# Optimization experiments

Hardware: AMD Instinct MI355X
Metric: run time of the kernel (lower is better)

The kernel has to match this reference:

```python
import jax, jax.numpy as jnp
import numpy as np

MASK_VALUE = -1000000.0

def setup_inputs() -> dict:
    key = jax.random.key(0)
    ks = jax.random.split(key, 8)
    B, Lq, Lk = 8, 128, 512
    Dq = Dk = H = Dv = 256
    queries = jax.random.normal(ks[0], (B, Lq, Dq), dtype=jnp.float32)
    keys = jax.random.normal(ks[1], (B, Lk, Dk), dtype=jnp.float32)
    values = jax.random.normal(ks[2], (B, Lk, Dv), dtype=jnp.float32)
    valid_lens = jax.random.randint(ks[3], (B,), 1, Lk + 1).astype(jnp.int32)
    # Learned parameters (stored as (in, out) so x @ W matches torch Linear)
    Wq = jax.random.normal(ks[4], (Dq, H), dtype=jnp.float32) / np.sqrt(Dq)
    Wk = jax.random.normal(ks[5], (Dk, H), dtype=jnp.float32) / np.sqrt(Dk)
    wv = jax.random.normal(ks[6], (H,), dtype=jnp.float32) / np.sqrt(H)
    return {"queries": queries, "keys": keys, "values": values,
            "valid_lens": valid_lens, "Wq": Wq, "Wk": Wk, "wv": wv}

def reference(queries, keys, values, valid_lens, Wq, Wk, wv):
    # projections
    q = jnp.einsum('bqd,dh->bqh', queries, Wq)   # (B, Lq, H)
    k = jnp.einsum('bkd,dh->bkh', keys, Wk)      # (B, Lk, H)
    # additive score: tanh(q_i + k_j) . w_v  -> (B, Lq, Lk)
    features = jnp.tanh(q[:, :, None, :] + k[:, None, :, :])  # (B, Lq, Lk, H)
    scores = jnp.einsum('bqkh,h->bqk', features, wv)
    # masked softmax over k axis; masked positions set to -1e6 (as in torch src)
    Lk = keys.shape[1]
    mask = jnp.arange(Lk)[None, None, :] >= valid_lens[:, None, None]  # (B,1,Lk)
    scores = jnp.where(mask, MASK_VALUE, scores)
    attn = jax.nn.softmax(scores, axis=-1)
    # dropout p=0.0 -> identity
    return jnp.einsum('bqk,bkv->bqv', attn, values)  # (B, Lq, Dv)
```

## Files before the change

### kernel.cpp

```cpp
#include <hip/hip_runtime.h>
#include <hip/hip_bf16.h>


#define SCALE_2LOG2E 2.885390081777927f
#define LOG2E        1.4426950408889634f
#define NEG_BIG     -1.0e30f

__device__ __forceinline__ float fast_exp2(float x) {
#if __has_builtin(__builtin_amdgcn_exp2f)
    return __builtin_amdgcn_exp2f(x);
#else
    return exp2f(x);
#endif
}
__device__ __forceinline__ float fast_rcp(float x) {
#if __has_builtin(__builtin_amdgcn_rcpf)
    return __builtin_amdgcn_rcpf(x);
#else
    return __fdividef(1.0f, x);
#endif
}

__global__ __launch_bounds__(256) void proj_kernel(
    const float* __restrict__ queries, const float* __restrict__ keys,
    const float* __restrict__ Wq, const float* __restrict__ Wk,
    const int* __restrict__ valid_lens,
    float* __restrict__ qproj, float* __restrict__ kproj)
{
    const int mt = blockIdx.y, nt = blockIdx.x;
    const float* X; const float* W; float* P; int row0;
    if (mt < 16) { X = queries; W = Wq; P = qproj; row0 = mt * 64; }
    else {
        const int kr = mt * 64 - 1024;
        const int b = kr >> 9, loc = kr & 511;
        if (loc >= valid_lens[b]) return;
        X = keys; W = Wk; P = kproj; row0 = kr;
    }
    const int t  = threadIdx.x;
    const int tx = t & 15, ty = t >> 4;
    const int ar = t >> 2, ac = t & 3;
    const int br = t >> 4, bc = t & 15;
    const int n0 = nt * 64;

    __shared__ float as[16][68];
    __shared__ float bs[16][68];

    const float* Aptr = X + (size_t)(row0 + ar) * 256 + ac * 4;
    const float* Bptr = W + (size_t)br * 256 + n0 + bc * 4;

    float4 av = *(const float4*)Aptr;
    float4 bv = *(const float4*)Bptr;

    float acc[4][4];
#pragma unroll
    for (int i = 0; i < 4; ++i)
#pragma unroll
        for (int j = 0; j < 4; ++j) acc[i][j] = 0.f;

    for (int ch = 0; ch < 16; ++ch) {
        __syncthreads();
        as[ac * 4 + 0][ar] = av.x;
        as[ac * 4 + 1][ar] = av.y;
        as[ac * 4 + 2][ar] = av.z;
        as[ac * 4 + 3][ar] = av.w;
        *(float4*)&bs[br][bc * 4] = bv;
        __syncthreads();
        if (ch < 15) {
            av = *(const float4*)(Aptr + (ch + 1) * 16);
            bv = *(const float4*)(Bptr + (size_t)(ch + 1) * 16 * 256);
        }
#pragma unroll
        for (int kk = 0; kk < 16; ++kk) {
            const float4 af = *(const float4*)&as[kk][ty * 4];
            const float4 bf = *(const float4*)&bs[kk][tx * 4];
            acc[0][0] += af.x * bf.x; acc[0][1] += af.x * bf.y;
            acc[0][2] += af.x * bf.z; acc[0][3] += af.x * bf.w;
            acc[1][0] += af.y * bf.x; acc[1][1] += af.y * bf.y;
            acc[1][2] += af.y * bf.z; acc[1][3] += af.y * bf.w;
            acc[2][0] += af.z * bf.x; acc[2][1] += af.z * bf.y;
            acc[2][2] += af.z * bf.z; acc[2][3] += af.z * bf.w;
            acc[3][0] += af.w * bf.x; acc[3][1] += af.w * bf.y;
            acc[3][2] += af.w * bf.z; acc[3][3] += af.w * bf.w;
        }
    }
#pragma unroll
    for (int i = 0; i < 4; ++i) {
        float4 o;
        o.x = acc[i][0] * SCALE_2LOG2E; o.y = acc[i][1] * SCALE_2LOG2E;
        o.z = acc[i][2] * SCALE_2LOG2E; o.w = acc[i][3] * SCALE_2LOG2E;
        *(float4*)(P + (size_t)(row0 + ty * 4 + i) * 256 + n0 + tx * 4) = o;
    }
}

__global__ __launch_bounds__(256) void score_kernel(
    const float* __restrict__ qproj,
    const float* __restrict__ kproj,
    const float* __restrict__ wv,
    const int*   __restrict__ valid_lens,
    float* __restrict__ scores)
{
    const int b  = blockIdx.z;
    const int vlen = valid_lens[b];
    const int k0 = blockIdx.x * 16;
    if (k0 >= vlen) return;
    const int q0 = blockIdx.y * 16;
    const int t  = threadIdx.x;

    __shared__ float qs[16][260];
    __shared__ float ks[16][260];
    __shared__ float wl[256];

    {
        const float4* qsrc = (const float4*)(qproj + (size_t)(b * 128 + q0) * 256);
        const float4* ksrc = (const float4*)(kproj + ((size_t)b * 512 + k0) * 256);
        for (int i = t; i < 1024; i += 256) {
            *(float4*)&qs[i >> 6][(i & 63) * 4] = qsrc[i];
            *(float4*)&ks[i >> 6][(i & 63) * 4] = ksrc[i];
        }
        if (t < 64) *(float4*)&wl[t * 4] = ((const float4*)wv)[t];
    }
    __syncthreads();

    const int tx = t & 15, ty = t >> 4;
    float acc = 0.f;
#pragma unroll 8
    for (int h0 = 0; h0 < 256; h0 += 4) {
        const float4 qf = *(const float4*)&qs[ty][h0];
        const float4 kf = *(const float4*)&ks[tx][h0];
        const float4 wf = *(const float4*)&wl[h0];
        float a, r;
        a = qf.x + kf.x; r = fast_rcp(fast_exp2(a) + 1.f);
        acc += wf.x * (1.f - 2.f * r);
        a = qf.y + kf.y; r = fast_rcp(fast_exp2(a) + 1.f);
        acc += wf.y * (1.f - 2.f * r);
        a = qf.z + kf.z; r = fast_rcp(fast_exp2(a) + 1.f);
        acc += wf.z * (1.f - 2.f * r);
        a = qf.w + kf.w; r = fast_rcp(fast_exp2(a) + 1.f);
        acc += wf.w * (1.f - 2.f * r);
    }
    if (k0 + tx < vlen)
        scores[(size_t)(b * 128 + q0 + ty) * 512 + k0 + tx] = acc;
}

__global__ __launch_bounds__(256) void softmax_pv_kernel(
    const float* __restrict__ scores,
    const float* __restrict__ values,
    const int*   __restrict__ valid_lens,
    float* __restrict__ out)
{
    __shared__ float attn[4][512];
    const int b = blockIdx.y, q0 = blockIdx.x * 4;
    const int t = threadIdx.x, w = t >> 6, lane = t & 63;
    const int vlen = valid_lens[b];
    const int row = q0 + w;

    const float* srow = scores + (size_t)(b * 128 + row) * 512;
    float sv[8];
#pragma unroll
    for (int j = 0; j < 8; ++j) {
        const int k = lane + 64 * j;
        sv[j] = (k < vlen) ? srow[k] : NEG_BIG;
    }

    float m = sv[0];
#pragma unroll
    for (int j = 1; j < 8; ++j) m = fmaxf(m, sv[j]);
#pragma unroll
    for (int o = 1; o < 64; o <<= 1) m = fmaxf(m, __shfl_xor(m, o));

    float sum = 0.f;
#pragma unroll
    for (int j = 0; j < 8; ++j) {
        sv[j] = fast_exp2((sv[j] - m) * LOG2E);
        sum += sv[j];
    }
#pragma unroll
    for (int o = 1; o < 64; o <<= 1) sum += __shfl_xor(sum, o);
    const float rs = fast_rcp(sum);

#pragma unroll
    for (int j = 0; j < 8; ++j) attn[w][lane + 64 * j] = sv[j] * rs;

    const float* V = values + (size_t)b * 512 * 256 + lane * 4;
    float4 acc = {0.f, 0.f, 0.f, 0.f};
#pragma unroll 4
    for (int k = 0; k < vlen; ++k) {
        const float a = attn[w][k];
        const float4 v4 = *(const float4*)(V + (size_t)k * 256);
        acc.x += a * v4.x; acc.y += a * v4.y;
        acc.z += a * v4.z; acc.w += a * v4.w;
    }
    *(float4*)(out + (size_t)(b * 128 + row) * 256 + lane * 4) = acc;
}

extern "C" void kernel_launch(void* const* d_in, const int* in_sizes, int n_in,
                              void* d_out, int out_size, void* d_ws, size_t ws_size,
                              hipStream_t stream) {
    const float* queries = (const float*)d_in[0];
    const float* keys    = (const float*)d_in[1];
    const float* values  = (const float*)d_in[2];
    const int*   vlens   = (const int*)  d_in[3];
    const float* Wq      = (const float*)d_in[4];
    const float* Wk      = (const float*)d_in[5];
    const float* wv      = (const float*)d_in[6];
    float* out = (float*)d_out;

    float* qproj  = (float*)d_ws;
    float* kproj  = qproj + 1024 * 256;
    float* scores = kproj + 4096 * 256;

    proj_kernel<<<dim3(4, 80), 256, 0, stream>>>(queries, keys, Wq, Wk,
                                                 vlens, qproj, kproj);
    score_kernel<<<dim3(32, 8, 8), 256, 0, stream>>>(qproj, kproj, wv,
                                                     vlens, scores);
    softmax_pv_kernel<<<dim3(32, 8), 256, 0, stream>>>(scores, values,
                                                       vlens, out);
}
```

Baseline: 148.7 us.

## Hoist tanh affine terms out of score loop and split PV over key halves

In the score kernel, tanh(x) = 1 - 2/(e^{2x}+1) is rearranged so the constant sum of wv is computed once per block with a wave reduction. The inner loop then only accumulates wv*rcp(exp2+1), which saves a few ALU ops per element. The softmax/PV kernel now handles 2 rows per block instead of 4, with two waves per row each covering half the keys, combined through shared memory. It also processes 4 keys per step using vectorized attention reads. This doubles the block count and adds parallelism for the memory-bound PV phase, at the cost of computing each row's softmax twice and adding a block sync.

Measured after the change: 141.5 us. 1.05x faster.

```diff
diff --git a/kernel.cpp b/kernel.cpp
--- a/kernel.cpp
+++ b/kernel.cpp
@@ -121,6 +121,14 @@
     }
     __syncthreads();
 
+    float wsum;
+    {
+        const float4 wq = *(const float4*)&wl[(t & 63) * 4];
+        wsum = wq.x + wq.y + wq.z + wq.w;
+#pragma unroll
+        for (int o = 1; o < 64; o <<= 1) wsum += __shfl_xor(wsum, o);
+    }
+
     const int tx = t & 15, ty = t >> 4;
     float acc = 0.f;
 #pragma unroll 8
@@ -128,18 +136,13 @@
         const float4 qf = *(const float4*)&qs[ty][h0];
         const float4 kf = *(const float4*)&ks[tx][h0];
         const float4 wf = *(const float4*)&wl[h0];
-        float a, r;
-        a = qf.x + kf.x; r = fast_rcp(fast_exp2(a) + 1.f);
-        acc += wf.x * (1.f - 2.f * r);
-        a = qf.y + kf.y; r = fast_rcp(fast_exp2(a) + 1.f);
-        acc += wf.y * (1.f - 2.f * r);
-        a = qf.z + kf.z; r = fast_rcp(fast_exp2(a) + 1.f);
-        acc += wf.z * (1.f - 2.f * r);
-        a = qf.w + kf.w; r = fast_rcp(fast_exp2(a) + 1.f);
-        acc += wf.w * (1.f - 2.f * r);
+        acc += wf.x * fast_rcp(fast_exp2(qf.x + kf.x) + 1.f);
+        acc += wf.y * fast_rcp(fast_exp2(qf.y + kf.y) + 1.f);
+        acc += wf.z * fast_rcp(fast_exp2(qf.z + kf.z) + 1.f);
+        acc += wf.w * fast_rcp(fast_exp2(qf.w + kf.w) + 1.f);
     }
     if (k0 + tx < vlen)
-        scores[(size_t)(b * 128 + q0 + ty) * 512 + k0 + tx] = acc;
+        scores[(size_t)(b * 128 + q0 + ty) * 512 + k0 + tx] = wsum - 2.f * acc;
 }
 
 __global__ __launch_bounds__(256) void softmax_pv_kernel(
@@ -148,11 +151,12 @@
     const int*   __restrict__ valid_lens,
     float* __restrict__ out)
 {
-    __shared__ float attn[4][512];
-    const int b = blockIdx.y, q0 = blockIdx.x * 4;
+    __shared__ float attn[2][512];
+    __shared__ float pout[2][256];
+    const int b = blockIdx.y, q0 = blockIdx.x * 2;
     const int t = threadIdx.x, w = t >> 6, lane = t & 63;
+    const int rr = w & 1, half = w >> 1, row = q0 + rr;
     const int vlen = valid_lens[b];
-    const int row = q0 + w;
 
     const float* srow = scores + (size_t)(b * 128 + row) * 512;
     float sv[8];
@@ -179,18 +183,40 @@
     const float rs = fast_rcp(sum);
 
 #pragma unroll
-    for (int j = 0; j < 8; ++j) attn[w][lane + 64 * j] = sv[j] * rs;
-
+    for (int j = 0; j < 4; ++j) {
+        const int jj = half * 4 + j;
+        attn[rr][lane + 64 * jj] = sv[jj] * rs;
+    }
+
+    const int vl16 = (vlen + 15) & ~15;
+    const int kbeg = half * 256;
+    const int kend = min(vl16, kbeg + 256);
     const float* V = values + (size_t)b * 512 * 256 + lane * 4;
+
     float4 acc = {0.f, 0.f, 0.f, 0.f};
-#pragma unroll 4
-    for (int k = 0; k < vlen; ++k) {
-        const float a = attn[w][k];
-        const float4 v4 = *(const float4*)(V + (size_t)k * 256);
-        acc.x += a * v4.x; acc.y += a * v4.y;
-        acc.z += a * v4.z; acc.w += a * v4.w;
-    }
-    *(float4*)(out + (size_t)(b * 128 + row) * 256 + lane * 4) = acc;
+    for (int k0 = kbeg; k0 < kend; k0 += 16) {
+#pragma unroll
+        for (int g = 0; g < 4; ++g) {
+            const int kk = k0 + g * 4;
+            const float4 aq = *(const float4*)&attn[rr][kk];
+            const float4 v0 = *(const float4*)(V + (size_t)(kk + 0) * 256);
+            const float4 v1 = *(const float4*)(V + (size_t)(kk + 1) * 256);
+            const float4 v2 = *(const float4*)(V + (size_t)(kk + 2) * 256);
+            const float4 v3 = *(const float4*)(V + (size_t)(kk + 3) * 256);
+            acc.x += aq.x * v0.x + aq.y * v1.x + aq.z * v2.x + aq.w * v3.x;
+            acc.y += aq.x * v0.y + aq.y * v1.y + aq.z * v2.y + aq.w * v3.y;
+            acc.z += aq.x * v0.z + aq.y * v1.z + aq.z * v2.z + aq.w * v3.z;
+            acc.w += aq.x * v0.w + aq.y * v1.w + aq.z * v2.w + aq.w * v3.w;
+        }
+    }
+
+    if (half) *(float4*)&pout[rr][lane * 4] = acc;
+    __syncthreads();
+    if (!half) {
+        const float4 p = *(const float4*)&pout[rr][lane * 4];
+        acc.x += p.x; acc.y += p.y; acc.z += p.z; acc.w += p.w;
+        *(float4*)(out + (size_t)(b * 128 + row) * 256 + lane * 4) = acc;
+    }
 }
 
 extern "C" void kernel_launch(void* const* d_in, const int* in_sizes, int n_in,
@@ -213,6 +239,6 @@
                                                  vlens, qproj, kproj);
     score_kernel<<<dim3(32, 8, 8), 256, 0, stream>>>(qproj, kproj, wv,
                                                      vlens, scores);
-    softmax_pv_kernel<<<dim3(32, 8), 256, 0, stream>>>(scores, values,
+    softmax_pv_kernel<<<dim3(64, 8), 256, 0, stream>>>(scores, values,
                                                        vlens, out);
 }
```
